# Kernel optimization log

Measured on AMD Instinct MI355X. Metric: run time of the kernel, lower is better.

The kernel has to match this reference:

```python
import jax, jax.numpy as jnp
import numpy as np

B, S, D = 2, 2048, 2048
NH, NKV, HD = 16, 4, 128
ROPE_BASE = 10000.0
NEG = -1e9


def _rope_tables(seq_len, dim):
    inv_freq = 1.0 / ROPE_BASE ** (jnp.arange(0, dim, 2, dtype=jnp.float32) / dim)
    t = jnp.arange(seq_len, dtype=jnp.float32)
    freqs = jnp.outer(t, inv_freq)                      # [S, dim/2]
    return jnp.cos(freqs), jnp.sin(freqs)


def _apply_rope(x, cos, sin):
    # x: [B, S, H, HD]; interleaved-pair rotation matching the original module
    x1 = x[..., ::2]
    x2 = x[..., 1::2]
    c = cos[None, :, None, :]
    s = sin[None, :, None, :]
    out1 = x1 * c - x2 * s
    out2 = x1 * s + x2 * c
    return jnp.stack([out1, out2], axis=-1).reshape(x.shape)


def setup_inputs() -> dict:
    key = jax.random.key(0)
    ks = jax.random.split(key, 5)
    x = jax.random.normal(ks[0], (B, S, D), dtype=jnp.float32)
    # causal additive mask [1, 1, S, S]
    causal = jnp.tril(jnp.ones((S, S), dtype=jnp.bool_))
    mask = jnp.where(causal, 0.0, NEG).astype(jnp.float32)[None, None]
    Wq = jax.random.normal(ks[1], (D, NH * HD), dtype=jnp.float32) * (D ** -0.5)
    Wk = jax.random.normal(ks[2], (D, NKV * HD), dtype=jnp.float32) * (D ** -0.5)
    Wv = jax.random.normal(ks[3], (D, NKV * HD), dtype=jnp.float32) * (D ** -0.5)
    Wo = jax.random.normal(ks[4], (NH * HD, D), dtype=jnp.float32) * ((NH * HD) ** -0.5)
    return {"x": x, "mask": mask, "Wq": Wq, "Wk": Wk, "Wv": Wv, "Wo": Wo}


def reference(x, mask, Wq, Wk, Wv, Wo):
    b, s, _ = x.shape
    q = (x @ Wq).reshape(b, s, NH, HD)
    k = (x @ Wk).reshape(b, s, NKV, HD)
    v = (x @ Wv).reshape(b, s, NKV, HD)

    cos, sin = _rope_tables(s, HD)
    q = _apply_rope(q, cos, sin)
    k = _apply_rope(k, cos, sin)

    rep = NH // NKV
    k = jnp.repeat(k, rep, axis=2)                       # [b, s, NH, HD]
    v = jnp.repeat(v, rep, axis=2)

    q = q.transpose(0, 2, 1, 3)                          # [b, NH, s, HD]
    k = k.transpose(0, 2, 1, 3)
    v = v.transpose(0, 2, 1, 3)

    scores = jnp.einsum('bhqd,bhkd->bhqk', q, k) / jnp.sqrt(jnp.float32(HD))
    scores = scores + mask
    attn = jax.nn.softmax(scores, axis=-1)
    out = jnp.einsum('bhqk,bhkd->bhqd', attn, v)
    out = out.transpose(0, 2, 1, 3).reshape(b, s, NH * HD)
    return out @ Wo
```

## Files before the change

### kernel.cpp

```cpp
#include <hip/hip_runtime.h>
#include <stdint.h>

#define B_    2
#define S_    2048
#define D_    2048
#define NH_   16
#define NKV_  4
#define HD_   128
#define M_    (B_*S_)
#define NQKV_ 3072

typedef __bf16 bf16x8 __attribute__((ext_vector_type(8)));
typedef float  f32x4  __attribute__((ext_vector_type(4)));

__device__ __forceinline__ unsigned short f2bf(float f) {
    unsigned int u = __float_as_uint(f);
    u += 0x7fffu + ((u >> 16) & 1u);
    return (unsigned short)(u >> 16);
}

__device__ __forceinline__ unsigned short cvt_bf(float f) {
    __bf16 b = (__bf16)f;
    return *(unsigned short*)&b;
}

__device__ __forceinline__ void async_cp16(const unsigned short* g, unsigned short* l) {
    __builtin_amdgcn_global_load_lds((const __attribute__((address_space(1))) void*)g,
                                     (__attribute__((address_space(3))) void*)l, 16, 0, 0);
}

__global__ void cast_x(const float* __restrict__ x, unsigned short* __restrict__ xb) {
    int idx = blockIdx.x * 256 + threadIdx.x;
    float4 v = ((const float4*)x)[idx];
    unsigned int lo = (unsigned int)f2bf(v.x) | ((unsigned int)f2bf(v.y) << 16);
    unsigned int hi = (unsigned int)f2bf(v.z) | ((unsigned int)f2bf(v.w) << 16);
    ((uint2*)xb)[idx] = make_uint2(lo, hi);
}

__global__ void transpose_cast(const float* __restrict__ src,
                               unsigned short* __restrict__ dst, int ncols) {
    __shared__ float tile[32][33];
    int tx = threadIdx.x, ty = threadIdx.y;
    int n0 = blockIdx.x * 32, k0 = blockIdx.y * 32;
#pragma unroll
    for (int i = 0; i < 4; i++) {
        int k = k0 + ty + i * 8;
        tile[ty + i * 8][tx] = src[(long)k * ncols + n0 + tx];
    }
    __syncthreads();
#pragma unroll
    for (int i = 0; i < 4; i++) {
        int n = n0 + ty + i * 8;
        dst[(long)n * 2048 + k0 + tx] = f2bf(tile[tx][ty + i * 8]);
    }
}

__global__ void rope_tables(float2* __restrict__ ctab) {
    int gid = blockIdx.x * 256 + threadIdx.x;
    int s = gid >> 6, i = gid & 63;
    float inv = exp2f(-(float)i * 0.20762050593046014f);
    float ang = (float)s * inv;
    float sn, cs; sincosf(ang, &sn, &cs);
    ctab[gid] = make_float2(cs, sn);
}


__device__ __forceinline__ bf16x8 lds_frag(const unsigned short* hb, int r, int ks, int quad) {
    int p = (r * 128 + ks * 64 + quad * 16) ^ ((r & 4) << 3);
    return *(const bf16x8*)((const char*)hb + p);
}

__device__ __forceinline__ void stage_half(const unsigned short* g, int Kel,
                                           unsigned short* lhalf, int wid, int lane) {
#pragma unroll
    for (int i = 0; i < 2; i++) {
        int chunk = wid * 2 + i;
        int o = chunk * 1024 + lane * 16;
        int row = o >> 7;
        int cb = (o & 127) ^ ((row & 4) << 3);
        async_cp16((const unsigned short*)((const char*)g + (size_t)row * Kel * 2 + cb),
                   lhalf + chunk * 512);
    }
}

template<int MB, int NB>
__device__ __forceinline__ void cluster(f32x4 (*acc)[4], bf16x8 (*a)[2], bf16x8 (*b)[2]) {
    __builtin_amdgcn_sched_barrier(0);
    __builtin_amdgcn_s_barrier();
    asm volatile("s_waitcnt lgkmcnt(0)" ::: "memory");
    __builtin_amdgcn_sched_barrier(0);
    __builtin_amdgcn_s_setprio(1);
#pragma unroll
    for (int ks = 0; ks < 2; ks++)
#pragma unroll
        for (int mi = 0; mi < 4; mi++)
#pragma unroll
            for (int ni = 0; ni < 2; ni++)
                acc[MB + mi][NB + ni] = __builtin_amdgcn_mfma_f32_16x16x32_bf16(
                    a[mi][ks], b[ni][ks], acc[MB + mi][NB + ni], 0, 0, 0);
    __builtin_amdgcn_s_setprio(0);
    __builtin_amdgcn_sched_barrier(0);
    __builtin_amdgcn_s_barrier();
    __builtin_amdgcn_sched_barrier(0);
}

__device__ __forceinline__ void gemm256_core(const unsigned short* __restrict__ A,
                                             const unsigned short* __restrict__ Bt,
                                             const int K, const int m0, const int n0,
                                             char* sm, f32x4 (*acc)[4]) {
    const int tid  = threadIdx.x;
    const int lane = tid & 63, wid = tid >> 6;
    const int quad = lane >> 4, l16 = lane & 15;
    const int wm = wid >> 2, wn = wid & 3;

    unsigned short* sA00 = (unsigned short*)(sm);
    unsigned short* sA01 = (unsigned short*)(sm + 16384);
    unsigned short* sA10 = (unsigned short*)(sm + 32768);
    unsigned short* sA11 = (unsigned short*)(sm + 49152);
    unsigned short* sB00 = (unsigned short*)(sm + 65536);
    unsigned short* sB01 = (unsigned short*)(sm + 81920);
    unsigned short* sB10 = (unsigned short*)(sm + 98304);
    unsigned short* sB11 = (unsigned short*)(sm + 114688);

    const unsigned short* A0 = A  + (size_t)m0 * K;
    const unsigned short* A1 = A  + (size_t)(m0 + 128) * K;
    const unsigned short* B0 = Bt + (size_t)n0 * K;
    const unsigned short* B1 = Bt + (size_t)(n0 + 128) * K;

    stage_half(A0,      K, sA00, wid, lane);
    stage_half(B1,      K, sB01, wid, lane);
    stage_half(A1,      K, sA01, wid, lane);
    stage_half(B0,      K, sB00, wid, lane);
    __builtin_amdgcn_sched_barrier(0);
    stage_half(A0 + 64, K, sA10, wid, lane);
    stage_half(B1 + 64, K, sB11, wid, lane);
    stage_half(A1 + 64, K, sA11, wid, lane);
    asm volatile("s_waitcnt vmcnt(6)" ::: "memory");
    __builtin_amdgcn_sched_barrier(0);
    __builtin_amdgcn_s_barrier();
    __builtin_amdgcn_sched_barrier(0);

    const int NIT = K >> 7;
    for (int j = 0; j < NIT; ++j) {
        const bool st = (j < NIT - 1);
        const int kof1 = (2 * j + 1) * 64;
        const int kof2 = (2 * j + 2) * 64;
        const int kof3 = (2 * j + 3) * 64;
        bf16x8 af[4][2], bA[2][2], bB[2][2];

#pragma unroll
        for (int mi = 0; mi < 4; mi++)
#pragma unroll
            for (int ks = 0; ks < 2; ks++)
                af[mi][ks] = lds_frag(sA00, wm * 64 + mi * 16 + l16, ks, quad);
#pragma unroll
        for (int ni = 0; ni < 2; ni++)
#pragma unroll
            for (int ks = 0; ks < 2; ks++)
                bA[ni][ks] = lds_frag(sB00, wn * 32 + ni * 16 + l16, ks, quad);
        stage_half(B0 + kof1, K, sB10, wid, lane);
        cluster<0, 0>(acc, af, bA);

#pragma unroll
        for (int ni = 0; ni < 2; ni++)
#pragma unroll
            for (int ks = 0; ks < 2; ks++)
                bB[ni][ks] = lds_frag(sB01, wn * 32 + ni * 16 + l16, ks, quad);
        if (st) stage_half(A0 + kof2, K, sA00, wid, lane);
        cluster<0, 2>(acc, af, bB);

#pragma unroll
        for (int mi = 0; mi < 4; mi++)
#pragma unroll
            for (int ks = 0; ks < 2; ks++)
                af[mi][ks] = lds_frag(sA01, wm * 64 + mi * 16 + l16, ks, quad);
        if (st) stage_half(B1 + kof2, K, sB01, wid, lane);
        cluster<4, 2>(acc, af, bB);

#pragma unroll
        for (int ni = 0; ni < 2; ni++)
#pragma unroll
            for (int ks = 0; ks < 2; ks++)
                bA[ni][ks] = lds_frag(sB00, wn * 32 + ni * 16 + l16, ks, quad);
        if (st) {
            stage_half(A1 + kof2, K, sA01, wid, lane);
            asm volatile("s_waitcnt vmcnt(6)" ::: "memory");
        } else {
            asm volatile("s_waitcnt vmcnt(0)" ::: "memory");
        }
        cluster<4, 0>(acc, af, bA);

#pragma unroll
        for (int mi = 0; mi < 4; mi++)
#pragma unroll
            for (int ks = 0; ks < 2; ks++)
                af[mi][ks] = lds_frag(sA10, wm * 64 + mi * 16 + l16, ks, quad);
#pragma unroll
        for (int ni = 0; ni < 2; ni++)
#pragma unroll
            for (int ks = 0; ks < 2; ks++)
                bA[ni][ks] = lds_frag(sB10, wn * 32 + ni * 16 + l16, ks, quad);
        if (st) stage_half(B0 + kof2, K, sB00, wid, lane);
        cluster<0, 0>(acc, af, bA);

#pragma unroll
        for (int ni = 0; ni < 2; ni++)
#pragma unroll
            for (int ks = 0; ks < 2; ks++)
                bB[ni][ks] = lds_frag(sB11, wn * 32 + ni * 16 + l16, ks, quad);
        if (st) stage_half(A0 + kof3, K, sA10, wid, lane);
        cluster<0, 2>(acc, af, bB);

#pragma unroll
        for (int mi = 0; mi < 4; mi++)
#pragma unroll
            for (int ks = 0; ks < 2; ks++)
                af[mi][ks] = lds_frag(sA11, wm * 64 + mi * 16 + l16, ks, quad);
        if (st) stage_half(B1 + kof3, K, sB11, wid, lane);
        cluster<4, 2>(acc, af, bB);

#pragma unroll
        for (int ni = 0; ni < 2; ni++)
#pragma unroll
            for (int ks = 0; ks < 2; ks++)
                bA[ni][ks] = lds_frag(sB10, wn * 32 + ni * 16 + l16, ks, quad);
        if (st) {
            stage_half(A1 + kof3, K, sA11, wid, lane);
            asm volatile("s_waitcnt vmcnt(6)" ::: "memory");
        }
        cluster<4, 0>(acc, af, bA);
    }
}

__global__ __launch_bounds__(512, 2) void gemm_qkv256(const unsigned short* __restrict__ A,
                                                      const unsigned short* __restrict__ Bt,
                                                      const float2* __restrict__ ctab,
                                                      unsigned short* __restrict__ Qr,
                                                      unsigned short* __restrict__ Kr,
                                                      unsigned short* __restrict__ Vrow) {
    extern __shared__ char sm[];
    const int m0 = blockIdx.y * 256, n0 = blockIdx.x * 256;
    f32x4 acc[8][4] = {};
    gemm256_core(A, Bt, D_, m0, n0, sm, acc);

    const int tid  = threadIdx.x;
    const int lane = tid & 63, wid = tid >> 6;
    const int quad = lane >> 4, l16 = lane & 15;
    const int wm = wid >> 2, wn = wid & 3;

    if (n0 < 2048) {
#pragma unroll
        for (int mt = 0; mt < 8; mt++) {
            int rowb = m0 + ((mt & 4) << 5) + wm * 64 + (mt & 3) * 16 + quad * 4;
#pragma unroll
            for (int nt = 0; nt < 4; nt++) {
                int col = n0 + ((nt & 2) << 6) + wn * 32 + (nt & 1) * 16 + l16;
                int h = col >> 7, d = col & 127;
#pragma unroll
                for (int r = 0; r < 4; r++) {
                    int row = rowb + r;
                    int s = row & 2047, b = row >> 11;
                    float2 cs = ctab[s * 64 + (d >> 1)];
                    float own = acc[mt][nt][r];
                    float other = __shfl_xor(own, 1);
                    float val = (d & 1) ? (other * cs.y + own * cs.x)
                                        : (own * cs.x - other * cs.y);
                    Qr[((size_t)(b * 16 + h) * 2048 + s) * 128 + d] = f2bf(val);
                }
            }
        }
    } else if (n0 < 2560) {
#pragma unroll
        for (int mt = 0; mt < 8; mt++) {
            int rowb = m0 + ((mt & 4) << 5) + wm * 64 + (mt & 3) * 16 + quad * 4;
#pragma unroll
            for (int nt = 0; nt < 4; nt++) {
                int col = n0 + ((nt & 2) << 6) + wn * 32 + (nt & 1) * 16 + l16;
                int kvh = (col - 2048) >> 7, d = col & 127;
#pragma unroll
                for (int r = 0; r < 4; r++) {
                    int row = rowb + r;
                    int s = row & 2047, b = row >> 11;
                    float2 cs = ctab[s * 64 + (d >> 1)];
                    float own = acc[mt][nt][r];
                    float other = __shfl_xor(own, 1);
                    float val = (d & 1) ? (other * cs.y + own * cs.x)
                                        : (own * cs.x - other * cs.y);
                    Kr[((size_t)(b * 4 + kvh) * 2048 + s) * 128 + d] = f2bf(val);
                }
            }
        }
    } else {
#pragma unroll
        for (int mt = 0; mt < 8; mt++) {
            int rowb = m0 + ((mt & 4) << 5) + wm * 64 + (mt & 3) * 16 + quad * 4;
#pragma unroll
            for (int nt = 0; nt < 4; nt++) {
                int col = n0 + ((nt & 2) << 6) + wn * 32 + (nt & 1) * 16 + l16;
#pragma unroll
                for (int r = 0; r < 4; r++)
                    Vrow[(size_t)(rowb + r) * 512 + (col - 2560)] = f2bf(acc[mt][nt][r]);
            }
        }
    }
}

__global__ __launch_bounds__(512, 2) void gemm_bt256(const unsigned short* __restrict__ A,
                                                     const unsigned short* __restrict__ Bt,
                                                     float* __restrict__ C) {
    extern __shared__ char sm[];
    const int m0 = blockIdx.y * 256, n0 = blockIdx.x * 256;
    f32x4 acc[8][4] = {};
    gemm256_core(A, Bt, NH_ * HD_, m0, n0, sm, acc);

    const int tid  = threadIdx.x;
    const int lane = tid & 63, wid = tid >> 6;
    const int quad = lane >> 4, l16 = lane & 15;
    const int wm = wid >> 2, wn = wid & 3;
#pragma unroll
    for (int mt = 0; mt < 8; mt++) {
        int rowb = m0 + ((mt & 4) << 5) + wm * 64 + (mt & 3) * 16 + quad * 4;
#pragma unroll
        for (int nt = 0; nt < 4; nt++) {
            int col = n0 + ((nt & 2) << 6) + wn * 32 + (nt & 1) * 16 + l16;
#pragma unroll
            for (int r = 0; r < 4; r++)
                C[(size_t)(rowb + r) * 2048 + col] = acc[mt][nt][r];
        }
    }
}

__global__ void v_trans_bf(const unsigned short* __restrict__ Vrow,
                           unsigned short* __restrict__ Vt) {
    __shared__ unsigned short tile[32][34];
    int tx = threadIdx.x, ty = threadIdx.y;
    int s0 = blockIdx.x * 32, d0 = blockIdx.y * 32;
    int bz = blockIdx.z;
    int b = bz >> 2, kvh = bz & 3;
#pragma unroll
    for (int i = 0; i < 4; i++) {
        int s = s0 + ty + i * 8;
        tile[ty + i * 8][tx] = Vrow[(long)(b * 2048 + s) * 512 + kvh * 128 + d0 + tx];
    }
    __syncthreads();
#pragma unroll
    for (int i = 0; i < 4; i++) {
        int d = d0 + ty + i * 8;
        Vt[((long)bz * 128 + d) * 2048 + s0 + tx] = tile[tx][ty + i * 8];
    }
}

__global__ __launch_bounds__(256) void attn_fwd(const unsigned short* __restrict__ Qr,
                                                const unsigned short* __restrict__ Kr,
                                                const unsigned short* __restrict__ Vt,
                                                unsigned short* __restrict__ O) {
    __shared__ char KsB[64 * 256];
    __shared__ char VsB[128 * 128];
    __shared__ unsigned short Ps[4][16][72];
    const int tid  = threadIdx.x;
    const int lane = tid & 63, wid = tid >> 6;
    const int quad = lane >> 4, l16 = lane & 15;
    const int pid = blockIdx.x, h = blockIdx.y, b = blockIdx.z;
    const int kvh = h >> 2;
    const unsigned short* qp = Qr + (long)(b * NH_ + h) * S_ * HD_;
    const char* kpB = (const char*)(Kr + (long)(b * NKV_ + kvh) * S_ * HD_);
    const char* vpB = (const char*)(Vt + (long)(b * NKV_ + kvh) * HD_ * S_);
    const float sc2 = 0.08838834764831845f * 1.4426950408889634f;

    const int wKb = (tid * 16) ^ ((((tid >> 4) & 7)) << 4);
    const int wVb = (tid * 16) ^ ((((tid >> 3) & 7)) << 4);
    const int gKb = tid * 16;
    const int gVb = (tid >> 3) * (S_ * 2) + (tid & 7) * 16;
    int kro[4], vro[2];
#pragma unroll
    for (int ks = 0; ks < 4; ks++)
        kro[ks] = l16 * 256 + ((ks * 64 + quad * 16) ^ ((l16 & 7) << 4));
#pragma unroll
    for (int ks2 = 0; ks2 < 2; ks2++)
        vro[ks2] = l16 * 128 + ((ks2 * 64 + quad * 16) ^ ((l16 & 7) << 4));

    bf16x8 ones;
#pragma unroll
    for (int i = 0; i < 8; i++) ones[i] = (__bf16)1.0f;

    for (int phase = 0; phase < 2; phase++) {
        const int qt = phase ? pid : 31 - pid;
        const int qw = qt * 64 + wid * 16;

        bf16x8 aq[4];
#pragma unroll
        for (int ks = 0; ks < 4; ks++)
            aq[ks] = *(const bf16x8*)&qp[(long)(qw + l16) * HD_ + ks * 32 + quad * 8];

        f32x4 o[8] = {};
        float mi[4], li[4];
#pragma unroll
        for (int r = 0; r < 4; r++) { mi[r] = -3.0e38f; li[r] = 0.f; }

        for (int kt = 0; kt <= qt; kt++) {
            const int kv0 = kt * 64;
            const char* kg = kpB + (size_t)kv0 * 256 + gKb;
            const char* vg = vpB + (size_t)kv0 * 2 + gVb;
            __syncthreads();
#pragma unroll
            for (int i = 0; i < 4; i++)
                *(uint4*)(KsB + wKb + i * 4096) = *(const uint4*)(kg + i * 4096);
#pragma unroll
            for (int i = 0; i < 4; i++)
                *(uint4*)(VsB + wVb + i * 4096) = *(const uint4*)(vg + (size_t)i * 32 * (S_ * 2));
            __syncthreads();

            f32x4 s[4] = {};
#pragma unroll
            for (int ks = 0; ks < 4; ks++)
#pragma unroll
                for (int nt = 0; nt < 4; nt++) {
                    bf16x8 kb = *(const bf16x8*)&KsB[kro[ks] + nt * 4096];
                    s[nt] = __builtin_amdgcn_mfma_f32_16x16x32_bf16(aq[ks], kb, s[nt], 0, 0, 0);
                }

            float mt4[4];
#pragma unroll
            for (int r = 0; r < 4; r++) mt4[r] = -3.0e38f;
            if (kv0 + 63 > qw) {
#pragma unroll
                for (int nt = 0; nt < 4; nt++) {
                    int kvp = kv0 + nt * 16 + l16;
#pragma unroll
                    for (int r = 0; r < 4; r++) {
                        float sv = s[nt][r] * sc2;
                        sv = (kvp <= qw + quad * 4 + r) ? sv : -1.0e30f;
                        s[nt][r] = sv;
                        mt4[r] = fmaxf(mt4[r], sv);
                    }
                }
            } else {
#pragma unroll
                for (int nt = 0; nt < 4; nt++)
#pragma unroll
                    for (int r = 0; r < 4; r++) {
                        float sv = s[nt][r] * sc2;
                        s[nt][r] = sv;
                        mt4[r] = fmaxf(mt4[r], sv);
                    }
            }
#pragma unroll
            for (int off = 1; off < 16; off <<= 1)
#pragma unroll
                for (int r = 0; r < 4; r++)
                    mt4[r] = fmaxf(mt4[r], __shfl_xor(mt4[r], off));

            bool grew = false;
#pragma unroll
            for (int r = 0; r < 4; r++) grew |= (mt4[r] > mi[r]);
            float al[4];
#pragma unroll
            for (int r = 0; r < 4; r++) {
                float mn = fmaxf(mi[r], mt4[r]);
                al[r] = exp2f(mi[r] - mn);
                mi[r] = mn;
            }
            if (__any(grew)) {
#pragma unroll
                for (int t = 0; t < 8; t++)
#pragma unroll
                    for (int r = 0; r < 4; r++) o[t][r] *= al[r];
            }
#pragma unroll
            for (int nt = 0; nt < 4; nt++)
#pragma unroll
                for (int r = 0; r < 4; r++)
                    s[nt][r] = exp2f(s[nt][r] - mi[r]);

#pragma unroll
            for (int nt = 0; nt < 4; nt++)
#pragma unroll
                for (int r = 0; r < 4; r++)
                    Ps[wid][quad * 4 + r][nt * 16 + l16] = cvt_bf(s[nt][r]);

            f32x4 sumf = {};
#pragma unroll
            for (int ks2 = 0; ks2 < 2; ks2++) {
                bf16x8 pa = *(const bf16x8*)&Ps[wid][l16][ks2 * 32 + quad * 8];
                sumf = __builtin_amdgcn_mfma_f32_16x16x32_bf16(pa, ones, sumf, 0, 0, 0);
#pragma unroll
                for (int vt = 0; vt < 8; vt++) {
                    bf16x8 vb = *(const bf16x8*)&VsB[vro[ks2] + vt * 2048];
                    o[vt] = __builtin_amdgcn_mfma_f32_16x16x32_bf16(pa, vb, o[vt], 0, 0, 0);
                }
            }
#pragma unroll
            for (int r = 0; r < 4; r++) li[r] = li[r] * al[r] + sumf[r];
        }

#pragma unroll
        for (int r = 0; r < 4; r++) {
            float inv_l = 1.0f / li[r];
            int qpos = qw + quad * 4 + r;
#pragma unroll
            for (int vt = 0; vt < 8; vt++) {
                float val = o[vt][r] * inv_l;
                O[(long)(b * S_ + qpos) * 2048 + h * 128 + vt * 16 + l16] = cvt_bf(val);
            }
        }
    }
}

extern "C" void kernel_launch(void* const* d_in, const int* in_sizes, int n_in,
                              void* d_out, int out_size, void* d_ws, size_t ws_size,
                              hipStream_t stream) {
    const float* x  = (const float*)d_in[0];
    const float* Wq = (const float*)d_in[2];
    const float* Wk = (const float*)d_in[3];
    const float* Wv = (const float*)d_in[4];
    const float* Wo = (const float*)d_in[5];

    char* ws = (char*)d_ws;
    unsigned short* xb    = (unsigned short*)(ws);
    unsigned short* Wqkvt = (unsigned short*)(ws + 16777216);
    unsigned short* Wot   = (unsigned short*)(ws + 29360128);
    float2*         ctab  = (float2*)        (ws + 37748736);
    unsigned short* Qr    = (unsigned short*)(ws + 38797312);
    unsigned short* Kr    = (unsigned short*)(ws + 55574528);
    unsigned short* Vrow  = (unsigned short*)(ws + 59768832);
    unsigned short* Vt    = (unsigned short*)(ws + 63963136);
    unsigned short* attn  = (unsigned short*)(ws + 68157440);

    static int attr_set = 0;
    if (!attr_set) {
        hipFuncSetAttribute(reinterpret_cast<const void*>(gemm_qkv256),
                            hipFuncAttributeMaxDynamicSharedMemorySize, 131072);
        hipFuncSetAttribute(reinterpret_cast<const void*>(gemm_bt256),
                            hipFuncAttributeMaxDynamicSharedMemorySize, 131072);
        attr_set = 1;
    }

    cast_x<<<8192, 256, 0, stream>>>(x, xb);
    dim3 tb(32, 8);
    transpose_cast<<<dim3(64, 64), tb, 0, stream>>>(Wq, Wqkvt, 2048);
    transpose_cast<<<dim3(16, 64), tb, 0, stream>>>(Wk, Wqkvt + 2048 * 2048, 512);
    transpose_cast<<<dim3(16, 64), tb, 0, stream>>>(Wv, Wqkvt + 2560 * 2048, 512);
    transpose_cast<<<dim3(64, 64), tb, 0, stream>>>(Wo, Wot, 2048);
    rope_tables<<<512, 256, 0, stream>>>(ctab);

    gemm_qkv256<<<dim3(12, 16), 512, 131072, stream>>>(xb, Wqkvt, ctab, Qr, Kr, Vrow);

    v_trans_bf<<<dim3(64, 4, 8), tb, 0, stream>>>(Vrow, Vt);

    attn_fwd<<<dim3(16, NH_, B_), 256, 0, stream>>>(Qr, Kr, Vt, attn);

    gemm_bt256<<<dim3(8, 16), 512, 131072, stream>>>(attn, Wot, (float*)d_out);
}
```

Baseline: 371.5 us.

## Double-buffer K/V tiles in shared memory for attention kernel

Splits the K and V shared-memory tiles into two buffers. The next tile's global loads are issued before the current tile's QK^T, softmax and PV compute, which drops one of the two block barriers per iteration. The goal is to hide global-load latency behind MFMA work. In exchange, K/V shared memory doubles, which may cut blocks per CU. Because the staging still goes through registers, the overlap depends on how the compiler schedules the LDS writes.

Result: slower. 422.7 us (+13.8%).

```diff
diff --git a/kernel.cpp b/kernel.cpp
--- a/kernel.cpp
+++ b/kernel.cpp
@@ -354,8 +354,10 @@
                                                 const unsigned short* __restrict__ Kr,
                                                 const unsigned short* __restrict__ Vt,
                                                 unsigned short* __restrict__ O) {
-    __shared__ char KsB[64 * 256];
-    __shared__ char VsB[128 * 128];
+    __shared__ char Ks0B[64 * 256];
+    __shared__ char Ks1B[64 * 256];
+    __shared__ char Vs0B[128 * 128];
+    __shared__ char Vs1B[128 * 128];
     __shared__ unsigned short Ps[4][16][72];
     const int tid  = threadIdx.x;
     const int lane = tid & 63, wid = tid >> 6;
@@ -383,6 +385,98 @@
 #pragma unroll
     for (int i = 0; i < 8; i++) ones[i] = (__bf16)1.0f;
 
+#define STAGE(KD, VD, kv0s) do {                                               \
+        const char* kg_ = kpB + (size_t)(kv0s) * 256 + gKb;                    \
+        const char* vg_ = vpB + (size_t)(kv0s) * 2 + gVb;                      \
+        _Pragma("unroll")                                                      \
+        for (int i_ = 0; i_ < 4; i_++)                                         \
+            *(uint4*)((KD) + wKb + i_ * 4096) = *(const uint4*)(kg_ + i_ * 4096); \
+        _Pragma("unroll")                                                      \
+        for (int i_ = 0; i_ < 4; i_++)                                         \
+            *(uint4*)((VD) + wVb + i_ * 4096) =                                \
+                *(const uint4*)(vg_ + (size_t)i_ * 32 * (S_ * 2));             \
+    } while (0)
+
+#define COMPUTE(KB, VB, kv0c) do {                                             \
+        f32x4 s_[4] = {};                                                      \
+        _Pragma("unroll")                                                      \
+        for (int ks_ = 0; ks_ < 4; ks_++)                                      \
+            _Pragma("unroll")                                                  \
+            for (int nt_ = 0; nt_ < 4; nt_++) {                                \
+                bf16x8 kb_ = *(const bf16x8*)&(KB)[kro[ks_] + nt_ * 4096];     \
+                s_[nt_] = __builtin_amdgcn_mfma_f32_16x16x32_bf16(aq[ks_], kb_, s_[nt_], 0, 0, 0); \
+            }                                                                  \
+        float mt4_[4];                                                         \
+        _Pragma("unroll")                                                      \
+        for (int r_ = 0; r_ < 4; r_++) mt4_[r_] = -3.0e38f;                    \
+        if ((kv0c) + 63 > qw) {                                                \
+            _Pragma("unroll")                                                  \
+            for (int nt_ = 0; nt_ < 4; nt_++) {                                \
+                int kvp_ = (kv0c) + nt_ * 16 + l16;                            \
+                _Pragma("unroll")                                              \
+                for (int r_ = 0; r_ < 4; r_++) {                               \
+                    float sv_ = s_[nt_][r_] * sc2;                             \
+                    sv_ = (kvp_ <= qw + quad * 4 + r_) ? sv_ : -1.0e30f;       \
+                    s_[nt_][r_] = sv_;                                         \
+                    mt4_[r_] = fmaxf(mt4_[r_], sv_);                           \
+                }                                                              \
+            }                                                                  \
+        } else {                                                               \
+            _Pragma("unroll")                                                  \
+            for (int nt_ = 0; nt_ < 4; nt_++)                                  \
+                _Pragma("unroll")                                              \
+                for (int r_ = 0; r_ < 4; r_++) {                               \
+                    float sv_ = s_[nt_][r_] * sc2;                             \
+                    s_[nt_][r_] = sv_;                                         \
+                    mt4_[r_] = fmaxf(mt4_[r_], sv_);                           \
+                }                                                              \
+        }                                                                      \
+        _Pragma("unroll")                                                      \
+        for (int off_ = 1; off_ < 16; off_ <<= 1)                              \
+            _Pragma("unroll")                                                  \
+            for (int r_ = 0; r_ < 4; r_++)                                     \
+                mt4_[r_] = fmaxf(mt4_[r_], __shfl_xor(mt4_[r_], off_));        \
+        bool grew_ = false;                                                    \
+        _Pragma("unroll")                                                      \
+        for (int r_ = 0; r_ < 4; r_++) grew_ |= (mt4_[r_] > mi[r_]);           \
+        float al_[4];                                                          \
+        _Pragma("unroll")                                                      \
+        for (int r_ = 0; r_ < 4; r_++) {                                       \
+            float mn_ = fmaxf(mi[r_], mt4_[r_]);                               \
+            al_[r_] = exp2f(mi[r_] - mn_);                                     \
+            mi[r_] = mn_;                                                      \
+        }                                                                      \
+        if (__any(grew_)) {                                                    \
+            _Pragma("unroll")                                                  \
+            for (int t_ = 0; t_ < 8; t_++)                                     \
+                _Pragma("unroll")                                              \
+                for (int r_ = 0; r_ < 4; r_++) o[t_][r_] *= al_[r_];           \
+        }                                                                      \
+        _Pragma("unroll")                                                      \
+        for (int nt_ = 0; nt_ < 4; nt_++)                                      \
+            _Pragma("unroll")                                                  \
+            for (int r_ = 0; r_ < 4; r_++)                                     \
+                s_[nt_][r_] = exp2f(s_[nt_][r_] - mi[r_]);                     \
+        _Pragma("unroll")                                                      \
+        for (int nt_ = 0; nt_ < 4; nt_++)                                      \
+            _Pragma("unroll")                                                  \
+            for (int r_ = 0; r_ < 4; r_++)                                     \
+                Ps[wid][quad * 4 + r_][nt_ * 16 + l16] = cvt_bf(s_[nt_][r_]);  \
+        f32x4 sumf_ = {};                                                      \
+        _Pragma("unroll")                                                      \
+        for (int ks2_ = 0; ks2_ < 2; ks2_++) {                                 \
+            bf16x8 pa_ = *(const bf16x8*)&Ps[wid][l16][ks2_ * 32 + quad * 8];  \
+            sumf_ = __builtin_amdgcn_mfma_f32_16x16x32_bf16(pa_, ones, sumf_, 0, 0, 0); \
+            _Pragma("unroll")                                                  \
+            for (int vt_ = 0; vt_ < 8; vt_++) {                                \
+                bf16x8 vb_ = *(const bf16x8*)&(VB)[vro[ks2_] + vt_ * 2048];    \
+                o[vt_] = __builtin_amdgcn_mfma_f32_16x16x32_bf16(pa_, vb_, o[vt_], 0, 0, 0); \
+            }                                                                  \
+        }                                                                      \
+        _Pragma("unroll")                                                      \
+        for (int r_ = 0; r_ < 4; r_++) li[r_] = li[r_] * al_[r_] + sumf_[r_];  \
+    } while (0)
+
     for (int phase = 0; phase < 2; phase++) {
         const int qt = phase ? pid : 31 - pid;
         const int qw = qt * 64 + wid * 16;
@@ -397,100 +491,18 @@
 #pragma unroll
         for (int r = 0; r < 4; r++) { mi[r] = -3.0e38f; li[r] = 0.f; }
 
-        for (int kt = 0; kt <= qt; kt++) {
-            const int kv0 = kt * 64;
-            const char* kg = kpB + (size_t)kv0 * 256 + gKb;
-            const char* vg = vpB + (size_t)kv0 * 2 + gVb;
+        STAGE(Ks0B, Vs0B, 0);
+        __syncthreads();
+
+        for (int kt = 0; kt <= qt; ) {
+            if (kt + 1 <= qt) STAGE(Ks1B, Vs1B, (kt + 1) * 64);
+            COMPUTE(Ks0B, Vs0B, kt * 64);
             __syncthreads();
-#pragma unroll
-            for (int i = 0; i < 4; i++)
-                *(uint4*)(KsB + wKb + i * 4096) = *(const uint4*)(kg + i * 4096);
-#pragma unroll
-            for (int i = 0; i < 4; i++)
-                *(uint4*)(VsB + wVb + i * 4096) = *(const uint4*)(vg + (size_t)i * 32 * (S_ * 2));
+            if (++kt > qt) break;
+            if (kt + 1 <= qt) STAGE(Ks0B, Vs0B, (kt + 1) * 64);
+            COMPUTE(Ks1B, Vs1B, kt * 64);
             __syncthreads();
-
-            f32x4 s[4] = {};
-#pragma unroll
-            for (int ks = 0; ks < 4; ks++)
-#pragma unroll
-                for (int nt = 0; nt < 4; nt++) {
-                    bf16x8 kb = *(const bf16x8*)&KsB[kro[ks] + nt * 4096];
-                    s[nt] = __builtin_amdgcn_mfma_f32_16x16x32_bf16(aq[ks], kb, s[nt], 0, 0, 0);
-                }
-
-            float mt4[4];
-#pragma unroll
-            for (int r = 0; r < 4; r++) mt4[r] = -3.0e38f;
-            if (kv0 + 63 > qw) {
-#pragma unroll
-                for (int nt = 0; nt < 4; nt++) {
-                    int kvp = kv0 + nt * 16 + l16;
-#pragma unroll
-                    for (int r = 0; r < 4; r++) {
-                        float sv = s[nt][r] * sc2;
-                        sv = (kvp <= qw + quad * 4 + r) ? sv : -1.0e30f;
-                        s[nt][r] = sv;
-                        mt4[r] = fmaxf(mt4[r], sv);
-                    }
-                }
-            } else {
-#pragma unroll
-                for (int nt = 0; nt < 4; nt++)
-#pragma unroll
-                    for (int r = 0; r < 4; r++) {
-                        float sv = s[nt][r] * sc2;
-                        s[nt][r] = sv;
-                        mt4[r] = fmaxf(mt4[r], sv);
-                    }
-            }
-#pragma unroll
-            for (int off = 1; off < 16; off <<= 1)
-#pragma unroll
-                for (int r = 0; r < 4; r++)
-                    mt4[r] = fmaxf(mt4[r], __shfl_xor(mt4[r], off));
-
-            bool grew = false;
-#pragma unroll
-            for (int r = 0; r < 4; r++) grew |= (mt4[r] > mi[r]);
-            float al[4];
-#pragma unroll
-            for (int r = 0; r < 4; r++) {
-                float mn = fmaxf(mi[r], mt4[r]);
-                al[r] = exp2f(mi[r] - mn);
-                mi[r] = mn;
-            }
-            if (__any(grew)) {
-#pragma unroll
-                for (int t = 0; t < 8; t++)
-#pragma unroll
-                    for (int r = 0; r < 4; r++) o[t][r] *= al[r];
-            }
-#pragma unroll
-            for (int nt = 0; nt < 4; nt++)
-#pragma unroll
-                for (int r = 0; r < 4; r++)
-                    s[nt][r] = exp2f(s[nt][r] - mi[r]);
-
-#pragma unroll
-            for (int nt = 0; nt < 4; nt++)
-#pragma unroll
-                for (int r = 0; r < 4; r++)
-                    Ps[wid][quad * 4 + r][nt * 16 + l16] = cvt_bf(s[nt][r]);
-
-            f32x4 sumf = {};
-#pragma unroll
-            for (int ks2 = 0; ks2 < 2; ks2++) {
-                bf16x8 pa = *(const bf16x8*)&Ps[wid][l16][ks2 * 32 + quad * 8];
-                sumf = __builtin_amdgcn_mfma_f32_16x16x32_bf16(pa, ones, sumf, 0, 0, 0);
-#pragma unroll
-                for (int vt = 0; vt < 8; vt++) {
-                    bf16x8 vb = *(const bf16x8*)&VsB[vro[ks2] + vt * 2048];
-                    o[vt] = __builtin_amdgcn_mfma_f32_16x16x32_bf16(pa, vb, o[vt], 0, 0, 0);
-                }
-            }
-#pragma unroll
-            for (int r = 0; r < 4; r++) li[r] = li[r] * al[r] + sumf[r];
+            ++kt;
         }
 
 #pragma unroll
@@ -504,6 +516,8 @@
             }
         }
     }
+#undef STAGE
+#undef COMPUTE
 }
 
 extern "C" void kernel_launch(void* const* d_in, const int* in_sizes, int n_in,
```

## Shrink output-projection GEMM tile to 128x256 to double grid size

Applied to the files above, without the earlier changes.

The output projection GEMM changes from 256x256 tiles (128 blocks) to 128x256 tiles (256 blocks), with its own hand-scheduled double-buffered pipeline that uses six LDS half-tiles and explicit vmcnt waits. The larger grid is meant to fill all of the GPU's compute units, where 128 blocks left many idle, and the smaller LDS footprint (96KB) may help occupancy. In exchange, each block reuses operands less, and the manual wait counts add a risk of ordering errors.

Result: faster. 346.3 us (-6.8%).

```diff
diff --git a/kernel.cpp b/kernel.cpp
--- a/kernel.cpp
+++ b/kernel.cpp
@@ -305,28 +305,120 @@
     }
 }
 
-__global__ __launch_bounds__(512, 2) void gemm_bt256(const unsigned short* __restrict__ A,
-                                                     const unsigned short* __restrict__ Bt,
-                                                     float* __restrict__ C) {
+__global__ __launch_bounds__(512, 2) void gemm_bt128x256(const unsigned short* __restrict__ A,
+                                                         const unsigned short* __restrict__ Bt,
+                                                         float* __restrict__ C) {
     extern __shared__ char sm[];
-    const int m0 = blockIdx.y * 256, n0 = blockIdx.x * 256;
-    f32x4 acc[8][4] = {};
-    gemm256_core(A, Bt, NH_ * HD_, m0, n0, sm, acc);
-
+    const int K = NH_ * HD_;
     const int tid  = threadIdx.x;
     const int lane = tid & 63, wid = tid >> 6;
     const int quad = lane >> 4, l16 = lane & 15;
     const int wm = wid >> 2, wn = wid & 3;
-#pragma unroll
-    for (int mt = 0; mt < 8; mt++) {
-        int rowb = m0 + ((mt & 4) << 5) + wm * 64 + (mt & 3) * 16 + quad * 4;
-#pragma unroll
-        for (int nt = 0; nt < 4; nt++) {
-            int col = n0 + ((nt & 2) << 6) + wn * 32 + (nt & 1) * 16 + l16;
-#pragma unroll
-            for (int r = 0; r < 4; r++)
-                C[(size_t)(rowb + r) * 2048 + col] = acc[mt][nt][r];
-        }
+    const int m0 = blockIdx.y * 128, n0 = blockIdx.x * 256;
+
+    unsigned short* sA0  = (unsigned short*)(sm);
+    unsigned short* sA1  = (unsigned short*)(sm + 16384);
+    unsigned short* sB00 = (unsigned short*)(sm + 32768);
+    unsigned short* sB01 = (unsigned short*)(sm + 49152);
+    unsigned short* sB10 = (unsigned short*)(sm + 65536);
+    unsigned short* sB11 = (unsigned short*)(sm + 81920);
+
+    const unsigned short* A0 = A  + (size_t)m0 * K;
+    const unsigned short* B0 = Bt + (size_t)n0 * K;
+    const unsigned short* B1 = Bt + (size_t)(n0 + 128) * K;
+
+    f32x4 acc[4][4] = {};
+
+    stage_half(A0,      K, sA0,  wid, lane);
+    stage_half(B0,      K, sB00, wid, lane);
+    stage_half(B1,      K, sB01, wid, lane);
+    __builtin_amdgcn_sched_barrier(0);
+    stage_half(A0 + 64, K, sA1,  wid, lane);
+    stage_half(B0 + 64, K, sB10, wid, lane);
+    asm volatile("s_waitcnt vmcnt(6)" ::: "memory");
+    __builtin_amdgcn_sched_barrier(0);
+    __builtin_amdgcn_s_barrier();
+    __builtin_amdgcn_sched_barrier(0);
+
+    const int NIT = K >> 7;
+    for (int j = 0; j < NIT; ++j) {
+        const bool st = (j < NIT - 1);
+        const int t1 = (2 * j + 1) * 64;
+        const int t2 = (2 * j + 2) * 64;
+        const int t3 = (2 * j + 3) * 64;
+        bf16x8 af[4][2], bb[2][2];
+
+#pragma unroll
+        for (int mi = 0; mi < 4; mi++)
+#pragma unroll
+            for (int ks = 0; ks < 2; ks++)
+                af[mi][ks] = lds_frag(sA0, wm * 64 + mi * 16 + l16, ks, quad);
+#pragma unroll
+        for (int ni = 0; ni < 2; ni++)
+#pragma unroll
+            for (int ks = 0; ks < 2; ks++)
+                bb[ni][ks] = lds_frag(sB00, wn * 32 + ni * 16 + l16, ks, quad);
+        stage_half(B1 + t1, K, sB11, wid, lane);
+        asm volatile("s_waitcnt vmcnt(6)" ::: "memory");
+        cluster<0, 0>(acc, af, bb);
+
+#pragma unroll
+        for (int ni = 0; ni < 2; ni++)
+#pragma unroll
+            for (int ks = 0; ks < 2; ks++)
+                bb[ni][ks] = lds_frag(sB01, wn * 32 + ni * 16 + l16, ks, quad);
+        if (st) {
+            stage_half(A0 + t2, K, sA0,  wid, lane);
+            stage_half(B0 + t2, K, sB00, wid, lane);
+            asm volatile("s_waitcnt vmcnt(6)" ::: "memory");
+        } else {
+            asm volatile("s_waitcnt vmcnt(2)" ::: "memory");
+        }
+        cluster<0, 2>(acc, af, bb);
+
+#pragma unroll
+        for (int mi = 0; mi < 4; mi++)
+#pragma unroll
+            for (int ks = 0; ks < 2; ks++)
+                af[mi][ks] = lds_frag(sA1, wm * 64 + mi * 16 + l16, ks, quad);
+#pragma unroll
+        for (int ni = 0; ni < 2; ni++)
+#pragma unroll
+            for (int ks = 0; ks < 2; ks++)
+                bb[ni][ks] = lds_frag(sB10, wn * 32 + ni * 16 + l16, ks, quad);
+        if (st) {
+            stage_half(B1 + t2, K, sB01, wid, lane);
+            asm volatile("s_waitcnt vmcnt(6)" ::: "memory");
+        } else {
+            asm volatile("s_waitcnt vmcnt(0)" ::: "memory");
+        }
+        cluster<0, 0>(acc, af, bb);
+
+#pragma unroll
+        for (int ni = 0; ni < 2; ni++)
+#pragma unroll
+            for (int ks = 0; ks < 2; ks++)
+                bb[ni][ks] = lds_frag(sB11, wn * 32 + ni * 16 + l16, ks, quad);
+        if (st) {
+            stage_half(A0 + t3, K, sA1,  wid, lane);
+            stage_half(B0 + t3, K, sB10, wid, lane);
+            asm volatile("s_waitcnt vmcnt(6)" ::: "memory");
+        }
+        cluster<0, 2>(acc, af, bb);
+    }
+
+#pragma unroll
+    for (int mi = 0; mi < 4; mi++) {
+        int rowb = m0 + wm * 64 + mi * 16 + quad * 4;
+#pragma unroll
+        for (int nb = 0; nb < 2; nb++)
+#pragma unroll
+            for (int ni = 0; ni < 2; ni++) {
+                int col = n0 + nb * 128 + wn * 32 + ni * 16 + l16;
+#pragma unroll
+                for (int r = 0; r < 4; r++)
+                    C[(size_t)(rowb + r) * 2048 + col] = acc[mi][nb * 2 + ni][r];
+            }
     }
 }
 
@@ -530,8 +622,8 @@
     if (!attr_set) {
         hipFuncSetAttribute(reinterpret_cast<const void*>(gemm_qkv256),
                             hipFuncAttributeMaxDynamicSharedMemorySize, 131072);
-        hipFuncSetAttribute(reinterpret_cast<const void*>(gemm_bt256),
-                            hipFuncAttributeMaxDynamicSharedMemorySize, 131072);
+        hipFuncSetAttribute(reinterpret_cast<const void*>(gemm_bt128x256),
+                            hipFuncAttributeMaxDynamicSharedMemorySize, 98304);
         attr_set = 1;
     }
 
@@ -549,5 +641,5 @@
 
     attn_fwd<<<dim3(16, NH_, B_), 256, 0, stream>>>(Qr, Kr, Vt, attn);
 
-    gemm_bt256<<<dim3(8, 16), 512, 131072, stream>>>(attn, Wot, (float*)d_out);
-}
+    gemm_bt128x256<<<dim3(8, 32), 512, 98304, stream>>>(attn, Wot, (float*)d_out);
+}
```
